# Kernel tuning notes

Measured on AMD Instinct MI355X. Metric: run time of the kernel, lower is better.

Reference implementation:

```python
import jax, jax.numpy as jnp
import numpy as np

_SAMPLING_EPS = 1e-5


def setup_inputs() -> dict:
    key = jax.random.key(0)
    ks = jax.random.split(key, 7)
    N, V, H = 256, 128000, 200  # num_seqs, vocab_size, output-history length
    logits = jax.random.normal(ks[0], (N, V), dtype=jnp.float32)
    output_tokens = jax.random.randint(ks[1], (N, H), 0, V, dtype=jnp.int32)
    presence_penalties = jax.random.uniform(ks[2], (N,), jnp.float32, 0.0, 2.0)
    frequency_penalties = jax.random.uniform(ks[3], (N,), jnp.float32, 0.0, 2.0)
    temperatures = jax.random.uniform(ks[4], (N,), jnp.float32, 0.5, 1.5)
    top_ps = jax.random.uniform(ks[5], (N,), jnp.float32, 0.5, 1.0)
    top_ks = jax.random.randint(ks[6], (N,), 1, 1000, dtype=jnp.int32)
    return {
        "logits": logits,
        "presence_penalties": presence_penalties,
        "frequency_penalties": frequency_penalties,
        "temperatures": temperatures,
        "top_ps": top_ps,
        "output_tokens": output_tokens,
        "top_ks": top_ks,
    }


def reference(logits, presence_penalties, frequency_penalties, temperatures,
              top_ps, output_tokens, top_ks):
    N, V = logits.shape

    # ---- _apply_penalties: bincount of previously generated tokens per row ----
    rows = jnp.arange(N)[:, None]  # [N,1] broadcast against [N,H] token ids
    bin_counts = jnp.zeros((N, V), logits.dtype).at[rows, output_tokens].add(1.0)
    # rows are skipped when both penalties are < eps (original builds an index list)
    active = ((presence_penalties >= _SAMPLING_EPS) |
              (frequency_penalties >= _SAMPLING_EPS))[:, None]
    presence_mask = (bin_counts > 0.0).astype(logits.dtype)
    penalty = (frequency_penalties[:, None] * bin_counts
               + presence_penalties[:, None] * presence_mask)
    logits = logits - jnp.where(active, penalty, jnp.zeros((), logits.dtype))

    # ---- temperature scaling + softmax ----
    logits = logits / temperatures[:, None]
    probs = jax.nn.softmax(logits, axis=-1)

    # ---- _apply_top_p_top_k: sort desc, cumsum, mask, unsort ----
    probs_idx = jnp.argsort(-probs, axis=-1)                    # descending order
    probs_sort = jnp.take_along_axis(probs, probs_idx, axis=-1)
    probs_sum = jnp.cumsum(probs_sort, axis=-1)
    top_p_mask = (probs_sum - probs_sort) > top_ps[:, None]     # exclusive cumsum > p
    probs_sort = jnp.where(top_p_mask, 0.0, probs_sort)
    top_k_mask = jnp.arange(V, dtype=top_ks.dtype)[None, :] >= top_ks[:, None]
    probs_sort = jnp.where(top_k_mask, 0.0, probs_sort)
    inv_idx = jnp.argsort(probs_idx, axis=-1)                   # unsort permutation
    filtered_probs = jnp.take_along_axis(probs_sort, inv_idx, axis=-1)
    return filtered_probs
```

## Files before the change

kernel.cpp:

```cpp
#include <hip/hip_runtime.h>
#include <stdint.h>

#define NB 8192
#define BSHIFT 19
#define HS 512
#define HM 511
#define CAP 4096
#define PCAP 2048
#define NRB 2048
#define NT 1024

typedef unsigned long long ull;

__device__ __forceinline__ unsigned mono_u32(float x) {
    unsigned b = __float_as_uint(x);
    return (b & 0x80000000u) ? ~b : (b | 0x80000000u);
}
__device__ __forceinline__ float inv_mono(unsigned u) {
    unsigned b = (u & 0x80000000u) ? (u & 0x7fffffffu) : ~u;
    return __uint_as_float(b);
}

__device__ __forceinline__ float compute_x(float l, int cnt,
                                           float pres, float freq, float t) {
    float pen = __fadd_rn(__fmul_rn(freq, (float)cnt), (cnt > 0) ? pres : 0.0f);
    return __fdiv_rn(__fsub_rn(l, pen), t);
}

__global__ __launch_bounds__(NT) void k_fused(
    const float* __restrict__ logits, const int* __restrict__ tokens,
    const float* __restrict__ pres_v, const float* __restrict__ freq_v,
    const float* __restrict__ temps, const float* __restrict__ topp_v,
    const int* __restrict__ topk_v, int V, int H, float* __restrict__ out)
{
    __shared__ __align__(16) char smem[(32 + 16 + 8 + 4) * 1024];
    unsigned* hc = (unsigned*)smem;
    ull* skey = (ull*)smem;
    char* regB = smem + 32 * 1024;
    float* se = (float*)regB;
    int* sct = (int*)regB;
    int* sct2 = (int*)(regB + 4 * 1024);
    ull* tmpc = (ull*)regB;
    char* regC = smem + 48 * 1024;
    float* bs1 = (float*)regC;
    float* bs2 = (float*)(regC + 4 * 1024);
    unsigned* rh = (unsigned*)regC;
    char* regD = smem + 56 * 1024;
    int* hkey = (int*)regD;
    int* hval = (int*)(regD + 2 * 1024);
    __shared__ float esum_s, corr_s;
    __shared__ int bstar_s, lcnt_s, rb_s, pcnt_s;

    int row = blockIdx.x, tid = threadIdx.x;
    for (int b = tid; b < NB; b += NT) hc[b] = 0u;
    if (tid == 0) { esum_s = 0.f; corr_s = 0.f; bstar_s = -1; lcnt_s = 0; rb_s = 0; pcnt_s = 0; }

    for (int i = tid; i < HS; i += NT) { hkey[i] = -1; hval[i] = 0; }
    __syncthreads();
    const int* trow = tokens + (size_t)row * H;
    for (int i = tid; i < H; i += NT) {
        int v = trow[i];
        unsigned h = ((unsigned)v * 2654435761u) >> 23;
        while (true) {
            int prev = atomicCAS(&hkey[h], -1, v);
            if (prev == -1 || prev == v) { atomicAdd(&hval[h], 1); break; }
            h = (h + 1) & HM;
        }
    }
    __syncthreads();

    float t = temps[row];
    float r = __fdiv_rn(1.0f, t);
    const float* lrow = logits + (size_t)row * V;
    const float4* l4p = (const float4*)lrow;
    int V4 = V >> 2;

    float es = 0.0f;
    int i = tid;
    for (; i + 7 * NT < V4; i += 8 * NT) {
        float4 arr[8];
#pragma unroll
        for (int q = 0; q < 8; ++q) arr[q] = l4p[i + q * NT];
#pragma unroll
        for (int q = 0; q < 8; ++q)
#pragma unroll
            for (int j = 0; j < 4; ++j) {
                float x = __fmul_rn((&arr[q].x)[j], r);
                atomicAdd(&hc[mono_u32(x) >> BSHIFT], 1u);
                es += __expf(x);
            }
    }
    for (; i < V4; i += NT) {
        float4 A = l4p[i];
#pragma unroll
        for (int j = 0; j < 4; ++j) {
            float x = __fmul_rn((&A.x)[j], r);
            atomicAdd(&hc[mono_u32(x) >> BSHIFT], 1u);
            es += __expf(x);
        }
    }
    for (int v = (V4 << 2) + tid; v < V; v += NT) {
        float x = __fmul_rn(lrow[v], r);
        atomicAdd(&hc[mono_u32(x) >> BSHIFT], 1u);
        es += __expf(x);
    }
    for (int off = 32; off; off >>= 1) es += __shfl_down(es, off);
    if ((tid & 63) == 0) atomicAdd(&esum_s, es);
    __syncthreads();

    float pres = pres_v[row], freq = freq_v[row];
    int active = (pres >= 1e-5f) || (freq >= 1e-5f);
    float corr = 0.0f;
    if (active) {
        for (int s = tid; s < HS; s += NT) {
            int v = hkey[s];
            if (v >= 0) {
                int c = hval[s];
                float l = lrow[v];
                float x0 = __fmul_rn(l, r);
                float xp = compute_x(l, c, pres, freq, t);
                unsigned b0 = mono_u32(x0) >> BSHIFT;
                unsigned bp = mono_u32(xp) >> BSHIFT;
                if (b0 != bp) { atomicSub(&hc[b0], 1u); atomicAdd(&hc[bp], 1u); }
                corr += __expf(xp) - __expf(x0);
            }
        }
    }
    for (int off = 32; off; off >>= 1) corr += __shfl_down(corr, off);
    if ((tid & 63) == 0) atomicAdd(&corr_s, corr);
    __syncthreads();

    const int BPT = NB / NT;
    int base = tid * BPT;
    int acc = 0;
#pragma unroll
    for (int q = BPT - 1; q >= 0; --q) { acc += (int)hc[base + q]; hc[base + q] = (unsigned)acc; }
    sct[tid] = acc;
    __syncthreads();
    {
        int* a = sct; int* b2 = sct2;
        for (int s = 1; s < NT; s <<= 1) {
            int v = a[tid] + ((tid + s < NT) ? a[tid + s] : 0);
            __syncthreads();
            b2[tid] = v;
            __syncthreads();
            int* tmp = a; a = b2; b2 = tmp;
        }
        int above = (tid < NT - 1) ? a[tid + 1] : 0;
        int k = topk_v[row];
        int best = -1;
#pragma unroll
        for (int q = BPT - 1; q >= 0; --q)
            if ((int)hc[base + q] + above >= k) { best = base + q; break; }
        if (best >= 0) atomicMax(&bstar_s, best);
    }
    __syncthreads();
    int bst = bstar_s - 2;
    if (bst < 0) bst = 0;
    float Sp = esum_s + corr_s;
    __syncthreads();

    float4* o4p = (float4*)(out + (size_t)row * V);
    const float4 z4 = make_float4(0.f, 0.f, 0.f, 0.f);
    i = tid;
    for (; i + 7 * NT < V4; i += 8 * NT) {
        float4 arr[8];
#pragma unroll
        for (int q = 0; q < 8; ++q) arr[q] = l4p[i + q * NT];
#pragma unroll
        for (int q = 0; q < 8; ++q) o4p[i + q * NT] = z4;
#pragma unroll
        for (int q = 0; q < 8; ++q) {
            int vb = (i + q * NT) << 2;
#pragma unroll
            for (int j = 0; j < 4; ++j) {
                float l = (&arr[q].x)[j];
                unsigned ua = mono_u32(__fmul_rn(l, r));
                if ((int)(ua >> BSHIFT) >= bst) {
                    unsigned ue = mono_u32(__fdiv_rn(l, t));
                    int pos = atomicAdd(&lcnt_s, 1);
                    if (pos < CAP)
                        skey[pos] = ((ull)ue << 32) | (unsigned)~(unsigned)(vb + j);
                }
            }
        }
    }
    for (; i < V4; i += NT) {
        float4 A = l4p[i];
        o4p[i] = z4;
#pragma unroll
        for (int j = 0; j < 4; ++j) {
            float l = (&A.x)[j];
            unsigned ua = mono_u32(__fmul_rn(l, r));
            if ((int)(ua >> BSHIFT) >= bst) {
                unsigned ue = mono_u32(__fdiv_rn(l, t));
                int pos = atomicAdd(&lcnt_s, 1);
                if (pos < CAP)
                    skey[pos] = ((ull)ue << 32) | (unsigned)~(unsigned)((i << 2) + j);
            }
        }
    }
    for (int v = (V4 << 2) + tid; v < V; v += NT) {
        float l = lrow[v];
        out[(size_t)row * V + v] = 0.0f;
        unsigned ua = mono_u32(__fmul_rn(l, r));
        if ((int)(ua >> BSHIFT) >= bst) {
            unsigned ue = mono_u32(__fdiv_rn(l, t));
            int pos = atomicAdd(&lcnt_s, 1);
            if (pos < CAP)
                skey[pos] = ((ull)ue << 32) | (unsigned)~(unsigned)v;
        }
    }
    __syncthreads();
    int count = lcnt_s; if (count > CAP) count = CAP;
    int k = topk_v[row];

    if (active) {
        for (int j = tid; j < count; j += NT) {
            unsigned idx = ~(unsigned)(skey[j] & 0xffffffffull);
            unsigned h = (idx * 2654435761u) >> 23;
            int c = 0;
            while (true) {
                int kk = hkey[h];
                if (kk == (int)idx) { c = hval[h]; break; }
                if (kk == -1) break;
                h = (h + 1) & HM;
            }
            if (c > 0) {
                float xp = compute_x(lrow[idx], c, pres, freq, t);
                skey[j] = ((ull)mono_u32(xp) << 32) | (unsigned)~idx;
            }
        }
    }
    __syncthreads();
    for (int g = tid; g < NRB; g += NT) rh[g] = 0u;
    __syncthreads();
    int gmin = bst << 6;
    for (int j = tid; j < count; j += NT) {
        unsigned u = (unsigned)(skey[j] >> 32);
        int rel = (int)(u >> 13) - gmin;
        rel = rel < 0 ? 0 : (rel > NRB - 1 ? NRB - 1 : rel);
        atomicAdd(&rh[rel], 1u);
    }
    __syncthreads();
    {
        int b2i = tid * 2;
        int a2 = (int)rh[b2i + 1];
        rh[b2i + 1] = (unsigned)a2;
        a2 += (int)rh[b2i];
        rh[b2i] = (unsigned)a2;
        sct[tid] = a2;
        __syncthreads();
        int* a = sct; int* b2 = sct2;
        for (int s = 1; s < NT; s <<= 1) {
            int v = a[tid] + ((tid + s < NT) ? a[tid + s] : 0);
            __syncthreads();
            b2[tid] = v;
            __syncthreads();
            int* tmp = a; a = b2; b2 = tmp;
        }
        int above = (tid < NT - 1) ? a[tid + 1] : 0;
        int best = -1;
        if ((int)rh[b2i + 1] + above >= k) best = b2i + 1;
        else if ((int)rh[b2i] + above >= k) best = b2i;
        if (best >= 0) atomicMax(&rb_s, best);
    }
    __syncthreads();
    int rb = rb_s;
    for (int j = tid; j < count; j += NT) {
        unsigned u = (unsigned)(skey[j] >> 32);
        int rel = (int)(u >> 13) - gmin;
        rel = rel < 0 ? 0 : (rel > NRB - 1 ? NRB - 1 : rel);
        if (rel >= rb) {
            int pos = atomicAdd(&pcnt_s, 1);
            if (pos < PCAP) tmpc[pos] = skey[j];
        }
    }
    __syncthreads();
    int count2 = pcnt_s;
    if (count2 <= PCAP) {
        for (int j = tid; j < count2; j += NT) skey[j] = tmpc[j];
        count = count2;
    }
    __syncthreads();

    int m = 1; while (m < count) m <<= 1;
    for (int j = count + tid; j < m; j += NT) skey[j] = 0ull;
    __syncthreads();
    for (int kk = 2; kk <= m; kk <<= 1) {
        for (int jj = kk >> 1; jj > 0; jj >>= 1) {
            for (int i2 = tid; i2 < m; i2 += NT) {
                int ixj = i2 ^ jj;
                if (ixj > i2) {
                    ull A = skey[i2], B = skey[ixj];
                    bool up = ((i2 & kk) != 0);
                    if ((A > B) == up) { skey[i2] = B; skey[ixj] = A; }
                }
            }
            __syncthreads();
        }
    }

    for (int j = tid; j < CAP; j += NT)
        se[j] = (j < count) ? __expf(inv_mono((unsigned)(skey[j] >> 32))) : 0.0f;
    __syncthreads();
    int j0 = tid << 2;
    float e0 = se[j0], e1 = se[j0 + 1], e2 = se[j0 + 2], e3 = se[j0 + 3];
    float c0 = e0, c1 = c0 + e1, c2 = c1 + e2, c3 = c2 + e3;
    bs1[tid] = c3;
    __syncthreads();
    float* a = bs1; float* b2 = bs2;
    for (int s = 1; s < NT; s <<= 1) {
        float v = a[tid] + ((tid >= s) ? a[tid - s] : 0.0f);
        __syncthreads();
        b2[tid] = v;
        __syncthreads();
        float* tmp = a; a = b2; b2 = tmp;
    }
    float pre = (tid > 0) ? a[tid - 1] : 0.0f;

    float pS = topp_v[row] * Sp;
    float inc[4] = {pre + c0, pre + c1, pre + c2, pre + c3};
    float ee[4] = {e0, e1, e2, e3};
#pragma unroll
    for (int q = 0; q < 4; ++q) {
        int j = j0 + q;
        if (j < count) {
            float e = ee[q];
            float excl = __fsub_rn(inc[q], e);
            if ((j < k) && (excl <= pS)) {
                unsigned idx = ~(unsigned)(skey[j] & 0xffffffffull);
                out[(size_t)row * V + idx] = __fdiv_rn(e, Sp);
            }
        }
    }
}

extern "C" void kernel_launch(void* const* d_in, const int* in_sizes, int n_in,
                              void* d_out, int out_size, void* d_ws, size_t ws_size,
                              hipStream_t stream) {
    const float* logits = (const float*)d_in[0];
    const float* pres   = (const float*)d_in[1];
    const float* freq   = (const float*)d_in[2];
    const float* temps  = (const float*)d_in[3];
    const float* topps  = (const float*)d_in[4];
    const int*   tokens = (const int*)d_in[5];
    const int*   topks  = (const int*)d_in[6];
    int N = in_sizes[1];
    int V = in_sizes[0] / N;
    int H = in_sizes[5] / N;
    float* out = (float*)d_out;

    k_fused<<<N, NT, 0, stream>>>(logits, tokens, pres, freq, temps, topps,
                                  topks, V, H, out);
}
```

Measured before the change: 295.8 us.

## Sample logits to estimate top-k threshold and fuse candidate collection into a single pass

A small strided sample of each row is histogrammed first to estimate a conservative top-k bucket threshold. The main pass then computes the exp-sum, zeroes the output and collects candidates above that threshold all at once, building the histogram only for those candidates. This removes the second full read of the logits row and most of the histogram atomics. A fallback rescans the full row when the estimate is too tight or the candidate buffer overflows, and the histogram is made coarser with a smaller shared-memory footprint.

Result: slower. 381.3 us (+28.9%).

```diff
diff --git a/kernel.cpp b/kernel.cpp
--- a/kernel.cpp
+++ b/kernel.cpp
@@ -1,8 +1,9 @@
 #include <hip/hip_runtime.h>
 #include <stdint.h>
 
-#define NB 8192
-#define BSHIFT 19
+#define NB 4096
+#define BSH 20
+#define RSH 14
 #define HS 512
 #define HM 511
 #define CAP 4096
@@ -27,36 +28,71 @@
     return __fdiv_rn(__fsub_rn(l, pen), t);
 }
 
+__device__ __forceinline__ int hash_lookup(const int* hkey, const int* hval, int v) {
+    unsigned h = ((unsigned)v * 2654435761u) >> 23;
+    while (true) {
+        int kk = hkey[h];
+        if (kk == v) return hval[h];
+        if (kk == -1) return 0;
+        h = (h + 1) & HM;
+    }
+}
+
+__device__ int suffix_cut(unsigned* hc, int* sct, int* sct2, int k, int tid, int* sh) {
+    if (tid == 0) *sh = -1;
+    const int BPT = NB / NT;
+    int base = tid * BPT;
+    int acc = 0;
+#pragma unroll
+    for (int q = BPT - 1; q >= 0; --q) { acc += (int)hc[base + q]; hc[base + q] = (unsigned)acc; }
+    sct[tid] = acc;
+    __syncthreads();
+    int* a = sct; int* b2 = sct2;
+    for (int s = 1; s < NT; s <<= 1) {
+        int v = a[tid] + ((tid + s < NT) ? a[tid + s] : 0);
+        __syncthreads();
+        b2[tid] = v;
+        __syncthreads();
+        int* tmp = a; a = b2; b2 = tmp;
+    }
+    int above = (tid < NT - 1) ? a[tid + 1] : 0;
+    int best = -1;
+#pragma unroll
+    for (int q = BPT - 1; q >= 0; --q)
+        if ((int)hc[base + q] + above >= k) { best = base + q; break; }
+    if (best >= 0) atomicMax(sh, best);
+    __syncthreads();
+    int r = *sh;
+    __syncthreads();
+    return r;
+}
+
 __global__ __launch_bounds__(NT) void k_fused(
     const float* __restrict__ logits, const int* __restrict__ tokens,
     const float* __restrict__ pres_v, const float* __restrict__ freq_v,
     const float* __restrict__ temps, const float* __restrict__ topp_v,
     const int* __restrict__ topk_v, int V, int H, float* __restrict__ out)
 {
-    __shared__ __align__(16) char smem[(32 + 16 + 8 + 4) * 1024];
-    unsigned* hc = (unsigned*)smem;
-    ull* skey = (ull*)smem;
-    char* regB = smem + 32 * 1024;
-    float* se = (float*)regB;
-    int* sct = (int*)regB;
-    int* sct2 = (int*)(regB + 4 * 1024);
-    ull* tmpc = (ull*)regB;
-    char* regC = smem + 48 * 1024;
-    float* bs1 = (float*)regC;
-    float* bs2 = (float*)(regC + 4 * 1024);
-    unsigned* rh = (unsigned*)regC;
-    char* regD = smem + 56 * 1024;
-    int* hkey = (int*)regD;
-    int* hval = (int*)(regD + 2 * 1024);
+    __shared__ ull skey[CAP];
+    __shared__ ull hreg[2048];
+    __shared__ int sct[NT], sct2[NT];
+    __shared__ int hkey[HS], hval[HS];
     __shared__ float esum_s, corr_s;
-    __shared__ int bstar_s, lcnt_s, rb_s, pcnt_s;
+    __shared__ int cut_s, lcnt_s, rb_s, pcnt_s;
+
+    unsigned* hc = (unsigned*)hreg;
+    unsigned* rh = (unsigned*)hreg;
+    ull* tmpc = hreg;
+    float* se = (float*)hreg;
+    float* bs1 = (float*)sct;
+    float* bs2 = (float*)sct2;
 
     int row = blockIdx.x, tid = threadIdx.x;
     for (int b = tid; b < NB; b += NT) hc[b] = 0u;
-    if (tid == 0) { esum_s = 0.f; corr_s = 0.f; bstar_s = -1; lcnt_s = 0; rb_s = 0; pcnt_s = 0; }
-
     for (int i = tid; i < HS; i += NT) { hkey[i] = -1; hval[i] = 0; }
-    __syncthreads();
+    if (tid == 0) { esum_s = 0.f; corr_s = 0.f; lcnt_s = 0; rb_s = 0; pcnt_s = 0; }
+    __syncthreads();
+
     const int* trow = tokens + (size_t)row * H;
     for (int i = tid; i < H; i += NT) {
         int v = trow[i];
@@ -67,49 +103,103 @@
             h = (h + 1) & HM;
         }
     }
-    __syncthreads();
 
     float t = temps[row];
     float r = __fdiv_rn(1.0f, t);
+    float pres = pres_v[row], freq = freq_v[row];
+    int active = (pres >= 1e-5f) || (freq >= 1e-5f);
+    int k = topk_v[row];
     const float* lrow = logits + (size_t)row * V;
     const float4* l4p = (const float4*)lrow;
     int V4 = V >> 2;
-
-    float es = 0.0f;
+    __syncthreads();
+
+    int S4 = V4 >> 4;
+    for (int s = tid; s < S4; s += NT) {
+        float4 A = l4p[(s << 4) + (s & 15)];
+#pragma unroll
+        for (int j = 0; j < 4; ++j)
+            atomicAdd(&hc[mono_u32(__fmul_rn((&A.x)[j], r)) >> BSH], 1u);
+    }
+    __syncthreads();
+    float ms = (S4 > 0) ? ((float)k * (float)(S4 << 2) / (float)V) : 0.0f;
+    int req = (int)(ms + 8.0f * sqrtf(ms) + 16.0f);
+    int bT = (S4 > 0) ? suffix_cut(hc, sct, sct2, req, tid, &cut_s) : 0;
+    int thr = bT - 1; if (thr < 0) thr = 0;
+    for (int b = tid; b < NB; b += NT) hc[b] = 0u;
+    __syncthreads();
+
+    float4* o4p = (float4*)(out + (size_t)row * V);
+    const float4 z4 = make_float4(0.f, 0.f, 0.f, 0.f);
+    float es0 = 0.f, es1 = 0.f, es2 = 0.f, es3 = 0.f;
     int i = tid;
     for (; i + 7 * NT < V4; i += 8 * NT) {
         float4 arr[8];
 #pragma unroll
         for (int q = 0; q < 8; ++q) arr[q] = l4p[i + q * NT];
 #pragma unroll
-        for (int q = 0; q < 8; ++q)
-#pragma unroll
-            for (int j = 0; j < 4; ++j) {
-                float x = __fmul_rn((&arr[q].x)[j], r);
-                atomicAdd(&hc[mono_u32(x) >> BSHIFT], 1u);
-                es += __expf(x);
-            }
+        for (int q = 0; q < 8; ++q) o4p[i + q * NT] = z4;
+#pragma unroll
+        for (int q = 0; q < 8; ++q) {
+            int vb = (i + q * NT) << 2;
+            float x0 = __fmul_rn(arr[q].x, r), x1 = __fmul_rn(arr[q].y, r);
+            float x2 = __fmul_rn(arr[q].z, r), x3 = __fmul_rn(arr[q].w, r);
+            es0 += __expf(x0); es1 += __expf(x1); es2 += __expf(x2); es3 += __expf(x3);
+            unsigned u0 = mono_u32(x0), u1 = mono_u32(x1);
+            unsigned u2 = mono_u32(x2), u3 = mono_u32(x3);
+            if ((int)(u0 >> BSH) >= thr) {
+                atomicAdd(&hc[u0 >> BSH], 1u);
+                int pos = atomicAdd(&lcnt_s, 1);
+                if (pos < CAP) skey[pos] = ((ull)u0 << 32) | (unsigned)~(unsigned)(vb);
+            }
+            if ((int)(u1 >> BSH) >= thr) {
+                atomicAdd(&hc[u1 >> BSH], 1u);
+                int pos = atomicAdd(&lcnt_s, 1);
+                if (pos < CAP) skey[pos] = ((ull)u1 << 32) | (unsigned)~(unsigned)(vb + 1);
+            }
+            if ((int)(u2 >> BSH) >= thr) {
+                atomicAdd(&hc[u2 >> BSH], 1u);
+                int pos = atomicAdd(&lcnt_s, 1);
+                if (pos < CAP) skey[pos] = ((ull)u2 << 32) | (unsigned)~(unsigned)(vb + 2);
+            }
+            if ((int)(u3 >> BSH) >= thr) {
+                atomicAdd(&hc[u3 >> BSH], 1u);
+                int pos = atomicAdd(&lcnt_s, 1);
+                if (pos < CAP) skey[pos] = ((ull)u3 << 32) | (unsigned)~(unsigned)(vb + 3);
+            }
+        }
     }
     for (; i < V4; i += NT) {
         float4 A = l4p[i];
+        o4p[i] = z4;
 #pragma unroll
         for (int j = 0; j < 4; ++j) {
             float x = __fmul_rn((&A.x)[j], r);
-            atomicAdd(&hc[mono_u32(x) >> BSHIFT], 1u);
-            es += __expf(x);
+            es0 += __expf(x);
+            unsigned u = mono_u32(x);
+            if ((int)(u >> BSH) >= thr) {
+                atomicAdd(&hc[u >> BSH], 1u);
+                int pos = atomicAdd(&lcnt_s, 1);
+                if (pos < CAP) skey[pos] = ((ull)u << 32) | (unsigned)~(unsigned)((i << 2) + j);
+            }
         }
     }
     for (int v = (V4 << 2) + tid; v < V; v += NT) {
         float x = __fmul_rn(lrow[v], r);
-        atomicAdd(&hc[mono_u32(x) >> BSHIFT], 1u);
-        es += __expf(x);
-    }
+        out[(size_t)row * V + v] = 0.0f;
+        es0 += __expf(x);
+        unsigned u = mono_u32(x);
+        if ((int)(u >> BSH) >= thr) {
+            atomicAdd(&hc[u >> BSH], 1u);
+            int pos = atomicAdd(&lcnt_s, 1);
+            if (pos < CAP) skey[pos] = ((ull)u << 32) | (unsigned)~(unsigned)v;
+        }
+    }
+    float es = (es0 + es1) + (es2 + es3);
     for (int off = 32; off; off >>= 1) es += __shfl_down(es, off);
     if ((tid & 63) == 0) atomicAdd(&esum_s, es);
     __syncthreads();
 
-    float pres = pres_v[row], freq = freq_v[row];
-    int active = (pres >= 1e-5f) || (freq >= 1e-5f);
     float corr = 0.0f;
     if (active) {
         for (int s = tid; s < HS; s += NT) {
@@ -119,9 +209,12 @@
                 float l = lrow[v];
                 float x0 = __fmul_rn(l, r);
                 float xp = compute_x(l, c, pres, freq, t);
-                unsigned b0 = mono_u32(x0) >> BSHIFT;
-                unsigned bp = mono_u32(xp) >> BSHIFT;
-                if (b0 != bp) { atomicSub(&hc[b0], 1u); atomicAdd(&hc[bp], 1u); }
+                int b0 = (int)(mono_u32(x0) >> BSH);
+                int bp = (int)(mono_u32(xp) >> BSH);
+                if (b0 != bp) {
+                    if (b0 >= thr) atomicSub(&hc[b0], 1u);
+                    if (bp >= thr) atomicAdd(&hc[bp], 1u);
+                }
                 corr += __expf(xp) - __expf(x0);
             }
         }
@@ -129,15 +222,83 @@
     for (int off = 32; off; off >>= 1) corr += __shfl_down(corr, off);
     if ((tid & 63) == 0) atomicAdd(&corr_s, corr);
     __syncthreads();
-
-    const int BPT = NB / NT;
-    int base = tid * BPT;
-    int acc = 0;
-#pragma unroll
-    for (int q = BPT - 1; q >= 0; --q) { acc += (int)hc[base + q]; hc[base + q] = (unsigned)acc; }
-    sct[tid] = acc;
+    int lraw = lcnt_s;
+    int count = lraw > CAP ? CAP : lraw;
+
+    for (int j = tid; j < count; j += NT) {
+        unsigned idx = ~(unsigned)(skey[j] & 0xffffffffull);
+        float l = lrow[idx];
+        int c = active ? hash_lookup(hkey, hval, (int)idx) : 0;
+        unsigned ue = (c > 0) ? mono_u32(compute_x(l, c, pres, freq, t))
+                              : mono_u32(__fdiv_rn(l, t));
+        skey[j] = ((ull)ue << 32) | (unsigned)~idx;
+    }
+    __syncthreads();
+
+    int bst = suffix_cut(hc, sct, sct2, k, tid, &cut_s);
+    bool ok = (bst >= thr + 1) && (lraw <= CAP);
+
+    if (!ok) {
+        for (int b = tid; b < NB; b += NT) hc[b] = 0u;
+        if (tid == 0) lcnt_s = 0;
+        __syncthreads();
+        for (int v = tid; v < V; v += NT)
+            atomicAdd(&hc[mono_u32(__fmul_rn(lrow[v], r)) >> BSH], 1u);
+        __syncthreads();
+        if (active) {
+            for (int s = tid; s < HS; s += NT) {
+                int v = hkey[s];
+                if (v >= 0) {
+                    int c = hval[s];
+                    float l = lrow[v];
+                    int b0 = (int)(mono_u32(__fmul_rn(l, r)) >> BSH);
+                    int bp = (int)(mono_u32(compute_x(l, c, pres, freq, t)) >> BSH);
+                    if (b0 != bp) { atomicSub(&hc[b0], 1u); atomicAdd(&hc[bp], 1u); }
+                }
+            }
+        }
+        __syncthreads();
+        bst = suffix_cut(hc, sct, sct2, k, tid, &cut_s);
+        int thr2 = bst - 1; if (thr2 < 0) thr2 = 0;
+        for (int v = tid; v < V; v += NT) {
+            unsigned u = mono_u32(__fmul_rn(lrow[v], r));
+            if ((int)(u >> BSH) >= thr2) {
+                int pos = atomicAdd(&lcnt_s, 1);
+                if (pos < CAP) skey[pos] = ((ull)u << 32) | (unsigned)~(unsigned)v;
+            }
+        }
+        __syncthreads();
+        count = lcnt_s > CAP ? CAP : lcnt_s;
+        for (int j = tid; j < count; j += NT) {
+            unsigned idx = ~(unsigned)(skey[j] & 0xffffffffull);
+            float l = lrow[idx];
+            int c = active ? hash_lookup(hkey, hval, (int)idx) : 0;
+            unsigned ue = (c > 0) ? mono_u32(compute_x(l, c, pres, freq, t))
+                                  : mono_u32(__fdiv_rn(l, t));
+            skey[j] = ((ull)ue << 32) | (unsigned)~idx;
+        }
+        __syncthreads();
+    }
+    float Sp = esum_s + corr_s;
+
+    for (int g = tid; g < NRB; g += NT) rh[g] = 0u;
+    __syncthreads();
+    int gmin = (bst - 1) << 6;
+    for (int j = tid; j < count; j += NT) {
+        unsigned u = (unsigned)(skey[j] >> 32);
+        int rel = (int)(u >> RSH) - gmin;
+        rel = rel < 0 ? 0 : (rel > NRB - 1 ? NRB - 1 : rel);
+        atomicAdd(&rh[rel], 1u);
+    }
     __syncthreads();
     {
+        int b2i = tid * 2;
+        int a2 = (int)rh[b2i + 1];
+        rh[b2i + 1] = (unsigned)a2;
+        a2 += (int)rh[b2i];
+        rh[b2i] = (unsigned)a2;
+        sct[tid] = a2;
+        __syncthreads();
         int* a = sct; int* b2 = sct2;
         for (int s = 1; s < NT; s <<= 1) {
             int v = a[tid] + ((tid + s < NT) ? a[tid + s] : 0);
@@ -147,119 +308,6 @@
             int* tmp = a; a = b2; b2 = tmp;
         }
         int above = (tid < NT - 1) ? a[tid + 1] : 0;
-        int k = topk_v[row];
-        int best = -1;
-#pragma unroll
-        for (int q = BPT - 1; q >= 0; --q)
-            if ((int)hc[base + q] + above >= k) { best = base + q; break; }
-        if (best >= 0) atomicMax(&bstar_s, best);
-    }
-    __syncthreads();
-    int bst = bstar_s - 2;
-    if (bst < 0) bst = 0;
-    float Sp = esum_s + corr_s;
-    __syncthreads();
-
-    float4* o4p = (float4*)(out + (size_t)row * V);
-    const float4 z4 = make_float4(0.f, 0.f, 0.f, 0.f);
-    i = tid;
-    for (; i + 7 * NT < V4; i += 8 * NT) {
-        float4 arr[8];
-#pragma unroll
-        for (int q = 0; q < 8; ++q) arr[q] = l4p[i + q * NT];
-#pragma unroll
-        for (int q = 0; q < 8; ++q) o4p[i + q * NT] = z4;
-#pragma unroll
-        for (int q = 0; q < 8; ++q) {
-            int vb = (i + q * NT) << 2;
-#pragma unroll
-            for (int j = 0; j < 4; ++j) {
-                float l = (&arr[q].x)[j];
-                unsigned ua = mono_u32(__fmul_rn(l, r));
-                if ((int)(ua >> BSHIFT) >= bst) {
-                    unsigned ue = mono_u32(__fdiv_rn(l, t));
-                    int pos = atomicAdd(&lcnt_s, 1);
-                    if (pos < CAP)
-                        skey[pos] = ((ull)ue << 32) | (unsigned)~(unsigned)(vb + j);
-                }
-            }
-        }
-    }
-    for (; i < V4; i += NT) {
-        float4 A = l4p[i];
-        o4p[i] = z4;
-#pragma unroll
-        for (int j = 0; j < 4; ++j) {
-            float l = (&A.x)[j];
-            unsigned ua = mono_u32(__fmul_rn(l, r));
-            if ((int)(ua >> BSHIFT) >= bst) {
-                unsigned ue = mono_u32(__fdiv_rn(l, t));
-                int pos = atomicAdd(&lcnt_s, 1);
-                if (pos < CAP)
-                    skey[pos] = ((ull)ue << 32) | (unsigned)~(unsigned)((i << 2) + j);
-            }
-        }
-    }
-    for (int v = (V4 << 2) + tid; v < V; v += NT) {
-        float l = lrow[v];
-        out[(size_t)row * V + v] = 0.0f;
-        unsigned ua = mono_u32(__fmul_rn(l, r));
-        if ((int)(ua >> BSHIFT) >= bst) {
-            unsigned ue = mono_u32(__fdiv_rn(l, t));
-            int pos = atomicAdd(&lcnt_s, 1);
-            if (pos < CAP)
-                skey[pos] = ((ull)ue << 32) | (unsigned)~(unsigned)v;
-        }
-    }
-    __syncthreads();
-    int count = lcnt_s; if (count > CAP) count = CAP;
-    int k = topk_v[row];
-
-    if (active) {
-        for (int j = tid; j < count; j += NT) {
-            unsigned idx = ~(unsigned)(skey[j] & 0xffffffffull);
-            unsigned h = (idx * 2654435761u) >> 23;
-            int c = 0;
-            while (true) {
-                int kk = hkey[h];
-                if (kk == (int)idx) { c = hval[h]; break; }
-                if (kk == -1) break;
-                h = (h + 1) & HM;
-            }
-            if (c > 0) {
-                float xp = compute_x(lrow[idx], c, pres, freq, t);
-                skey[j] = ((ull)mono_u32(xp) << 32) | (unsigned)~idx;
-            }
-        }
-    }
-    __syncthreads();
-    for (int g = tid; g < NRB; g += NT) rh[g] = 0u;
-    __syncthreads();
-    int gmin = bst << 6;
-    for (int j = tid; j < count; j += NT) {
-        unsigned u = (unsigned)(skey[j] >> 32);
-        int rel = (int)(u >> 13) - gmin;
-        rel = rel < 0 ? 0 : (rel > NRB - 1 ? NRB - 1 : rel);
-        atomicAdd(&rh[rel], 1u);
-    }
-    __syncthreads();
-    {
-        int b2i = tid * 2;
-        int a2 = (int)rh[b2i + 1];
-        rh[b2i + 1] = (unsigned)a2;
-        a2 += (int)rh[b2i];
-        rh[b2i] = (unsigned)a2;
-        sct[tid] = a2;
-        __syncthreads();
-        int* a = sct; int* b2 = sct2;
-        for (int s = 1; s < NT; s <<= 1) {
-            int v = a[tid] + ((tid + s < NT) ? a[tid + s] : 0);
-            __syncthreads();
-            b2[tid] = v;
-            __syncthreads();
-            int* tmp = a; a = b2; b2 = tmp;
-        }
-        int above = (tid < NT - 1) ? a[tid + 1] : 0;
         int best = -1;
         if ((int)rh[b2i + 1] + above >= k) best = b2i + 1;
         else if ((int)rh[b2i] + above >= k) best = b2i;
@@ -269,7 +317,7 @@
     int rb = rb_s;
     for (int j = tid; j < count; j += NT) {
         unsigned u = (unsigned)(skey[j] >> 32);
-        int rel = (int)(u >> 13) - gmin;
+        int rel = (int)(u >> RSH) - gmin;
         rel = rel < 0 ? 0 : (rel > NRB - 1 ? NRB - 1 : rel);
         if (rel >= rb) {
             int pos = atomicAdd(&pcnt_s, 1);
@@ -307,6 +355,7 @@
     int j0 = tid << 2;
     float e0 = se[j0], e1 = se[j0 + 1], e2 = se[j0 + 2], e3 = se[j0 + 3];
     float c0 = e0, c1 = c0 + e1, c2 = c1 + e2, c3 = c2 + e3;
+    __syncthreads();
     bs1[tid] = c3;
     __syncthreads();
     float* a = bs1; float* b2 = bs2;
```
